# Performance work log

Hardware: AMD Instinct MI355X
Metric: run time of the kernel (lower is better)

The kernel has to match this reference:

```python
import jax, jax.numpy as jnp
import numpy as np

NUM_NODES = 100000
EMB_DIM = 256
HID_DIM = 256
NUM_REL = 500
NUM_EDGES = 250000


def setup_inputs() -> dict:
    key = jax.random.key(0)
    ks = jax.random.split(key, 6)
    x = jax.random.normal(ks[0], (NUM_NODES, EMB_DIM), dtype=jnp.float32)
    edge_index = jax.random.randint(ks[1], (2, NUM_EDGES), 0, NUM_NODES, dtype=jnp.int64)
    edge_type = jax.random.randint(ks[2], (NUM_EDGES,), 0, NUM_REL, dtype=jnp.int64)
    # nn.Linear weights: shape [out, in]; _init_weights -> normal(0,1), bias zero
    W_head = jax.random.normal(ks[3], (HID_DIM, EMB_DIM), dtype=jnp.float32)
    b_head = jnp.zeros((HID_DIM,), dtype=jnp.float32)
    W_tail = jax.random.normal(ks[4], (HID_DIM, EMB_DIM), dtype=jnp.float32)
    b_tail = jnp.zeros((HID_DIM,), dtype=jnp.float32)
    rel_emb = jax.random.normal(ks[5], (NUM_REL, HID_DIM), dtype=jnp.float32)
    return {"x": x, "edge_index": edge_index, "edge_type": edge_type,
            "W_head": W_head, "b_head": b_head,
            "W_tail": W_tail, "b_tail": b_tail, "rel_emb": rel_emb}


def reference(x, edge_index, edge_type, W_head, b_head, W_tail, b_tail, rel_emb):
    # gcn == 'no' branch of DistMultNet.forward
    h_head = x[edge_index[0]] @ W_head.T + b_head          # [E, H]
    h_tail = x[edge_index[1]] @ W_tail.T + b_tail          # [E, H]
    h_rel = rel_emb[edge_type]                             # [E, H]
    scores = jnp.sum(h_head * h_rel * h_tail, axis=1)      # [E]
    return jax.nn.sigmoid(scores)
```

## Files before the change

### kernel.cpp

```cpp
#include <hip/hip_runtime.h>
#include <math.h>

#define EMB 256

typedef _Float16 half8 __attribute__((ext_vector_type(8)));
typedef float f32x4 __attribute__((ext_vector_type(4)));

__device__ __forceinline__ void gload_lds16(const void* gsrc, void* lds) {
    __builtin_amdgcn_global_load_lds(
        (const __attribute__((address_space(1))) void*)gsrc,
        (__attribute__((address_space(3))) void*)lds,
        16, 0, 0);
}

__device__ __forceinline__ void split8(const f32x4 a, const f32x4 b,
                                       half8& hi, half8& lo) {
#pragma unroll
    for (int i = 0; i < 4; ++i) {
        hi[i]     = (_Float16)a[i];
        lo[i]     = (_Float16)(a[i] - (float)hi[i]);
        hi[4 + i] = (_Float16)b[i];
        lo[4 + i] = (_Float16)(b[i] - (float)hi[4 + i]);
    }
}

__global__ void presplit_w(const float* __restrict__ Wh, const float* __restrict__ Wt,
                           _Float16* __restrict__ Whs, _Float16* __restrict__ Wts)
{
    const int g = blockIdx.x * 256 + threadIdx.x;
    const int m = g >> 5;
    const int cs = g & 31;
    const int c = cs >> 2, seg = cs & 3;
    const float* src = (m < 256) ? Wh : Wt;
    _Float16* dst    = (m < 256) ? Whs : Wts;
    const int r = m & 255;

    const float* s = src + (size_t)r * EMB + c * 32 + seg * 8;
    const f32x4 v0 = *(const f32x4*)s;
    const f32x4 v1 = *(const f32x4*)(s + 4);
    half8 hi, lo;
    split8(v0, v1, hi, lo);
    _Float16* d = dst + (size_t)r * 512 + c * 64;
    const int sw = r & 7;
    *(half8*)(d + ((seg       ^ sw) << 3)) = hi;
    *(half8*)(d + (((4 + seg) ^ sw) << 3)) = lo;
}

__global__ __launch_bounds__(256, 2)
void gemm_single(const float* __restrict__ X,
                 const _Float16* __restrict__ Whs, const _Float16* __restrict__ Wts,
                 const float* __restrict__ bh, const float* __restrict__ bt,
                 float* __restrict__ Hout, float* __restrict__ Tout,
                 int M, int nwg)
{
    __shared__ __align__(16) float    Af[2][128 * 32];
    __shared__ __align__(16) _Float16 Bf[2][128 * 64];

    const int fl = blockIdx.x;
    const int q = nwg >> 3, r = nwg & 7;
    const int xcd = fl & 7, ix = fl >> 3;
    const int wg = (xcd < r) ? xcd * (q + 1) + ix
                             : r * (q + 1) + (xcd - r) * q + ix;
    const int variant = wg & 3;
    const int m0 = (wg >> 2) << 7;
    const int n0 = (variant & 1) << 7;
    const int sel = variant >> 1;
    const _Float16* __restrict__ Ws = sel ? Wts : Whs;
    const float* __restrict__ bias  = sel ? bt : bh;
    float* __restrict__ OUT         = sel ? Tout : Hout;

    const int tid = threadIdx.x;
    const int lane = tid & 63;
    const int wv = tid >> 6;
    const int wm = (wv >> 1) << 6;
    const int wn = (wv & 1) << 6;
    const int l15 = lane & 15, l4 = lane >> 4;

    const int srow = tid >> 3;
    const int sg = tid & 7;
    int aSrcOff[4];
    const char* bSrc0 = (const char*)Ws + (size_t)(n0 + srow) * 1024 + sg * 16;
#pragma unroll
    for (int i = 0; i < 4; ++i) {
        const int row = srow + (i << 5);
        aSrcOff[i] = (sg ^ (row & 7)) << 4;
    }
    const int ldOff = srow * 128 + sg * 16;

    f32x4 acc[4][4];
#pragma unroll
    for (int i = 0; i < 4; ++i)
#pragma unroll
        for (int j = 0; j < 4; ++j) acc[i][j] = (f32x4){0.f, 0.f, 0.f, 0.f};

    auto STAGE = [&](int b, int c) {
        const int cb = c << 7;
#pragma unroll
        for (int i = 0; i < 4; ++i) {
            const int row = srow + (i << 5);
            const int gm = m0 + row;
            const int gmc = gm < M ? gm : M - 1;
            gload_lds16((const char*)X + (size_t)gmc * 1024 + cb + aSrcOff[i],
                        (char*)&Af[b][0] + ldOff + (i << 12));
            gload_lds16(bSrc0 + (size_t)i * 32768 + cb,
                        (char*)&Bf[b][0] + ldOff + (i << 12));
        }
    };

    STAGE(0, 0);
    __syncthreads();

    for (int c = 0; c < 8; ++c) {
        const int buf = c & 1;
        if (c < 7) STAGE(buf ^ 1, c + 1);

        const char* Ab = (const char*)&Af[buf][0];
        const char* Bb = (const char*)&Bf[buf][0];

        half8 ahh[4], ahl[4];
#pragma unroll
        for (int fi = 0; fi < 4; ++fi) {
            const int row = wm + fi * 16 + l15;
            const char* rb = Ab + row * 128;
            const f32x4 a0 = *(const f32x4*)(rb + (((l4 << 1)      ^ (row & 7)) << 4));
            const f32x4 a1 = *(const f32x4*)(rb + ((((l4 << 1) | 1) ^ (row & 7)) << 4));
            split8(a0, a1, ahh[fi], ahl[fi]);
        }
#pragma unroll
        for (int j = 0; j < 4; ++j) {
            const int n = wn + j * 16 + l15;
            const int n7 = n & 7;
            const char* nb = Bb + n * 128;
            const half8 bhh = *(const half8*)(nb + (((l4    ) ^ n7) << 4));
            const half8 bhl = *(const half8*)(nb + (((l4 + 4) ^ n7) << 4));
#pragma unroll
            for (int i = 0; i < 4; ++i) {
                acc[i][j] = __builtin_amdgcn_mfma_f32_16x16x32_f16(ahh[i], bhh, acc[i][j], 0, 0, 0);
                acc[i][j] = __builtin_amdgcn_mfma_f32_16x16x32_f16(ahh[i], bhl, acc[i][j], 0, 0, 0);
                acc[i][j] = __builtin_amdgcn_mfma_f32_16x16x32_f16(ahl[i], bhh, acc[i][j], 0, 0, 0);
            }
        }
        __syncthreads();
    }

    float bv[4];
#pragma unroll
    for (int j = 0; j < 4; ++j) bv[j] = bias[n0 + wn + j * 16 + l15];

#pragma unroll
    for (int i = 0; i < 4; ++i) {
        const int rbase = m0 + wm + i * 16 + l4 * 4;
#pragma unroll
        for (int rg = 0; rg < 4; ++rg) {
            const int gr = rbase + rg;
            if (gr < M) {
                float* dst = &OUT[(size_t)gr * EMB + n0 + wn];
#pragma unroll
                for (int j = 0; j < 4; ++j)
                    dst[j * 16 + l15] = acc[i][j][rg] + bv[j];
            }
        }
    }
}

__global__ __launch_bounds__(256)
void edge_score2(const float* __restrict__ H, const float* __restrict__ T,
                 const float* __restrict__ rel, const int* __restrict__ ei,
                 const int* __restrict__ et, float* __restrict__ out, int E)
{
    const int lane = threadIdx.x & 63;
    const int wid = threadIdx.x >> 6;
    const int e0 = (blockIdx.x * 4 + wid) * 2;
    if (e0 >= E) return;
    const bool two = (e0 + 1) < E;
    const int e1 = two ? e0 + 1 : e0;

    const int s0 = ei[e0], s1 = ei[e1];
    const int d0 = ei[E + e0], d1 = ei[E + e1];
    const int r0 = et[e0], r1 = et[e1];

    const int lo = lane * 4;
    const float4 h0 = *(const float4*)&H[(size_t)s0 * EMB + lo];
    const float4 h1 = *(const float4*)&H[(size_t)s1 * EMB + lo];
    const float4 t0 = *(const float4*)&T[(size_t)d0 * EMB + lo];
    const float4 t1 = *(const float4*)&T[(size_t)d1 * EMB + lo];
    const float4 g0 = *(const float4*)&rel[(size_t)r0 * EMB + lo];
    const float4 g1 = *(const float4*)&rel[(size_t)r1 * EMB + lo];

    float p0 = h0.x * g0.x * t0.x + h0.y * g0.y * t0.y
             + h0.z * g0.z * t0.z + h0.w * g0.w * t0.w;
    float p1 = h1.x * g1.x * t1.x + h1.y * g1.y * t1.y
             + h1.z * g1.z * t1.z + h1.w * g1.w * t1.w;
#pragma unroll
    for (int off = 32; off > 0; off >>= 1) {
        p0 += __shfl_xor(p0, off, 64);
        p1 += __shfl_xor(p1, off, 64);
    }
    if (lane == 0) {
        out[e0] = 1.0f / (1.0f + expf(-p0));
        if (two) out[e1] = 1.0f / (1.0f + expf(-p1));
    }
}

__global__ __launch_bounds__(256)
void edge_direct(const float* __restrict__ X, const int* __restrict__ ei,
                 const int* __restrict__ et,
                 const float* __restrict__ Wh, const float* __restrict__ bh,
                 const float* __restrict__ Wt, const float* __restrict__ bt,
                 const float* __restrict__ rel, float* __restrict__ out, int E)
{
    __shared__ float xsrc[EMB], xdst[EMB];
    __shared__ float red[256];
    const int e = blockIdx.x;
    const int tid = threadIdx.x;
    const int src = ei[e], dst = ei[E + e], r = et[e];

    xsrc[tid] = X[(size_t)src * EMB + tid];
    xdst[tid] = X[(size_t)dst * EMB + tid];
    __syncthreads();

    float ah = 0.f, at = 0.f;
    const float* wh = Wh + (size_t)tid * EMB;
    const float* wt = Wt + (size_t)tid * EMB;
#pragma unroll 8
    for (int k = 0; k < EMB; k += 4) {
        float4 w4 = *(const float4*)&wh[k];
        ah += w4.x * xsrc[k] + w4.y * xsrc[k + 1] + w4.z * xsrc[k + 2] + w4.w * xsrc[k + 3];
        float4 v4 = *(const float4*)&wt[k];
        at += v4.x * xdst[k] + v4.y * xdst[k + 1] + v4.z * xdst[k + 2] + v4.w * xdst[k + 3];
    }
    red[tid] = (ah + bh[tid]) * rel[(size_t)r * EMB + tid] * (at + bt[tid]);
    __syncthreads();
    for (int s2 = 128; s2 > 0; s2 >>= 1) {
        if (tid < s2) red[tid] += red[tid + s2];
        __syncthreads();
    }
    if (tid == 0) out[e] = 1.0f / (1.0f + expf(-red[0]));
}

extern "C" void kernel_launch(void* const* d_in, const int* in_sizes, int n_in,
                              void* d_out, int out_size, void* d_ws, size_t ws_size,
                              hipStream_t stream) {
    const float* x   = (const float*)d_in[0];
    const int*   ei  = (const int*)d_in[1];
    const int*   et  = (const int*)d_in[2];
    const float* Wh  = (const float*)d_in[3];
    const float* bh  = (const float*)d_in[4];
    const float* Wt  = (const float*)d_in[5];
    const float* bt  = (const float*)d_in[6];
    const float* rel = (const float*)d_in[7];
    float* out = (float*)d_out;

    const int M = in_sizes[0] / EMB;
    const int E = in_sizes[2];

    const size_t szHT = (size_t)2 * M * EMB * sizeof(float);
    const size_t szWs = (size_t)2 * 256 * 512 * sizeof(_Float16);

    if (ws_size >= szHT + szWs) {
        float* H = (float*)d_ws;
        float* T = H + (size_t)M * EMB;
        _Float16* Whs = (_Float16*)((char*)d_ws + szHT);
        _Float16* Wts = Whs + (size_t)256 * 512;

        presplit_w<<<64, 256, 0, stream>>>(Wh, Wt, Whs, Wts);
        const int mtiles = (M + 127) / 128;
        const int nwg = 4 * mtiles;
        gemm_single<<<nwg, 256, 0, stream>>>(x, Whs, Wts, bh, bt, H, T, M, nwg);
        edge_score2<<<(E + 7) / 8, 256, 0, stream>>>(H, T, rel, ei, et, out, E);
    } else {
        edge_direct<<<E, 256, 0, stream>>>(x, ei, et, Wh, bh, Wt, bt, rel, out, E);
    }
}
```

Measured before the change: 217.5 us.

## Load GEMM operands directly from global to registers, score four edges per wave

```diff
diff --git a/kernel.cpp b/kernel.cpp
--- a/kernel.cpp
+++ b/kernel.cpp
@@ -5,13 +5,6 @@
 
 typedef _Float16 half8 __attribute__((ext_vector_type(8)));
 typedef float f32x4 __attribute__((ext_vector_type(4)));
-
-__device__ __forceinline__ void gload_lds16(const void* gsrc, void* lds) {
-    __builtin_amdgcn_global_load_lds(
-        (const __attribute__((address_space(1))) void*)gsrc,
-        (__attribute__((address_space(3))) void*)lds,
-        16, 0, 0);
-}
 
 __device__ __forceinline__ void split8(const f32x4 a, const f32x4 b,
                                        half8& hi, half8& lo) {
@@ -40,22 +33,18 @@
     const f32x4 v1 = *(const f32x4*)(s + 4);
     half8 hi, lo;
     split8(v0, v1, hi, lo);
-    _Float16* d = dst + (size_t)r * 512 + c * 64;
-    const int sw = r & 7;
-    *(half8*)(d + ((seg       ^ sw) << 3)) = hi;
-    *(half8*)(d + (((4 + seg) ^ sw) << 3)) = lo;
-}
-
-__global__ __launch_bounds__(256, 2)
-void gemm_single(const float* __restrict__ X,
+    _Float16* d = dst + (size_t)r * 512 + c * 64 + seg * 8;
+    *(half8*)d        = hi;
+    *(half8*)(d + 32) = lo;
+}
+
+__global__ __launch_bounds__(256, 3)
+void gemm_direct(const float* __restrict__ X,
                  const _Float16* __restrict__ Whs, const _Float16* __restrict__ Wts,
                  const float* __restrict__ bh, const float* __restrict__ bt,
                  float* __restrict__ Hout, float* __restrict__ Tout,
                  int M, int nwg)
 {
-    __shared__ __align__(16) float    Af[2][128 * 32];
-    __shared__ __align__(16) _Float16 Bf[2][128 * 64];
-
     const int fl = blockIdx.x;
     const int q = nwg >> 3, r = nwg & 7;
     const int xcd = fl & 7, ix = fl >> 3;
@@ -76,16 +65,17 @@
     const int wn = (wv & 1) << 6;
     const int l15 = lane & 15, l4 = lane >> 4;
 
-    const int srow = tid >> 3;
-    const int sg = tid & 7;
-    int aSrcOff[4];
-    const char* bSrc0 = (const char*)Ws + (size_t)(n0 + srow) * 1024 + sg * 16;
-#pragma unroll
-    for (int i = 0; i < 4; ++i) {
-        const int row = srow + (i << 5);
-        aSrcOff[i] = (sg ^ (row & 7)) << 4;
-    }
-    const int ldOff = srow * 128 + sg * 16;
+    const float* aP[4];
+#pragma unroll
+    for (int fi = 0; fi < 4; ++fi) {
+        int row = m0 + wm + fi * 16 + l15;
+        if (row >= M) row = M - 1;
+        aP[fi] = X + (size_t)row * EMB + l4 * 8;
+    }
+    const _Float16* bP[4];
+#pragma unroll
+    for (int j = 0; j < 4; ++j)
+        bP[j] = Ws + (size_t)(n0 + wn + j * 16 + l15) * 512 + l4 * 8;
 
     f32x4 acc[4][4];
 #pragma unroll
@@ -93,54 +83,28 @@
 #pragma unroll
         for (int j = 0; j < 4; ++j) acc[i][j] = (f32x4){0.f, 0.f, 0.f, 0.f};
 
-    auto STAGE = [&](int b, int c) {
-        const int cb = c << 7;
-#pragma unroll
-        for (int i = 0; i < 4; ++i) {
-            const int row = srow + (i << 5);
-            const int gm = m0 + row;
-            const int gmc = gm < M ? gm : M - 1;
-            gload_lds16((const char*)X + (size_t)gmc * 1024 + cb + aSrcOff[i],
-                        (char*)&Af[b][0] + ldOff + (i << 12));
-            gload_lds16(bSrc0 + (size_t)i * 32768 + cb,
-                        (char*)&Bf[b][0] + ldOff + (i << 12));
+#pragma unroll
+    for (int c = 0; c < 8; ++c) {
+        half8 ah[4], al[4];
+#pragma unroll
+        for (int fi = 0; fi < 4; ++fi) {
+            const float* ap = aP[fi] + c * 32;
+            const f32x4 a0 = *(const f32x4*)ap;
+            const f32x4 a1 = *(const f32x4*)(ap + 4);
+            split8(a0, a1, ah[fi], al[fi]);
         }
-    };
-
-    STAGE(0, 0);
-    __syncthreads();
-
-    for (int c = 0; c < 8; ++c) {
-        const int buf = c & 1;
-        if (c < 7) STAGE(buf ^ 1, c + 1);
-
-        const char* Ab = (const char*)&Af[buf][0];
-        const char* Bb = (const char*)&Bf[buf][0];
-
-        half8 ahh[4], ahl[4];
-#pragma unroll
-        for (int fi = 0; fi < 4; ++fi) {
-            const int row = wm + fi * 16 + l15;
-            const char* rb = Ab + row * 128;
-            const f32x4 a0 = *(const f32x4*)(rb + (((l4 << 1)      ^ (row & 7)) << 4));
-            const f32x4 a1 = *(const f32x4*)(rb + ((((l4 << 1) | 1) ^ (row & 7)) << 4));
-            split8(a0, a1, ahh[fi], ahl[fi]);
-        }
 #pragma unroll
         for (int j = 0; j < 4; ++j) {
-            const int n = wn + j * 16 + l15;
-            const int n7 = n & 7;
-            const char* nb = Bb + n * 128;
-            const half8 bhh = *(const half8*)(nb + (((l4    ) ^ n7) << 4));
-            const half8 bhl = *(const half8*)(nb + (((l4 + 4) ^ n7) << 4));
+            const _Float16* bp = bP[j] + c * 64;
+            const half8 bh8 = *(const half8*)bp;
+            const half8 bl8 = *(const half8*)(bp + 32);
 #pragma unroll
             for (int i = 0; i < 4; ++i) {
-                acc[i][j] = __builtin_amdgcn_mfma_f32_16x16x32_f16(ahh[i], bhh, acc[i][j], 0, 0, 0);
-                acc[i][j] = __builtin_amdgcn_mfma_f32_16x16x32_f16(ahh[i], bhl, acc[i][j], 0, 0, 0);
-                acc[i][j] = __builtin_amdgcn_mfma_f32_16x16x32_f16(ahl[i], bhh, acc[i][j], 0, 0, 0);
+                acc[i][j] = __builtin_amdgcn_mfma_f32_16x16x32_f16(ah[i], bh8, acc[i][j], 0, 0, 0);
+                acc[i][j] = __builtin_amdgcn_mfma_f32_16x16x32_f16(ah[i], bl8, acc[i][j], 0, 0, 0);
+                acc[i][j] = __builtin_amdgcn_mfma_f32_16x16x32_f16(al[i], bh8, acc[i][j], 0, 0, 0);
             }
         }
-        __syncthreads();
     }
 
     float bv[4];
@@ -164,41 +128,46 @@
 }
 
 __global__ __launch_bounds__(256)
-void edge_score2(const float* __restrict__ H, const float* __restrict__ T,
+void edge_score4(const float* __restrict__ H, const float* __restrict__ T,
                  const float* __restrict__ rel, const int* __restrict__ ei,
                  const int* __restrict__ et, float* __restrict__ out, int E)
 {
     const int lane = threadIdx.x & 63;
     const int wid = threadIdx.x >> 6;
-    const int e0 = (blockIdx.x * 4 + wid) * 2;
-    if (e0 >= E) return;
-    const bool two = (e0 + 1) < E;
-    const int e1 = two ? e0 + 1 : e0;
-
-    const int s0 = ei[e0], s1 = ei[e1];
-    const int d0 = ei[E + e0], d1 = ei[E + e1];
-    const int r0 = et[e0], r1 = et[e1];
+    const int base = (blockIdx.x * 4 + wid) * 4;
+    if (base >= E) return;
+
+    int e[4];
+#pragma unroll
+    for (int u = 0; u < 4; ++u) {
+        int eu = base + u;
+        e[u] = eu < E ? eu : E - 1;
+    }
 
     const int lo = lane * 4;
-    const float4 h0 = *(const float4*)&H[(size_t)s0 * EMB + lo];
-    const float4 h1 = *(const float4*)&H[(size_t)s1 * EMB + lo];
-    const float4 t0 = *(const float4*)&T[(size_t)d0 * EMB + lo];
-    const float4 t1 = *(const float4*)&T[(size_t)d1 * EMB + lo];
-    const float4 g0 = *(const float4*)&rel[(size_t)r0 * EMB + lo];
-    const float4 g1 = *(const float4*)&rel[(size_t)r1 * EMB + lo];
-
-    float p0 = h0.x * g0.x * t0.x + h0.y * g0.y * t0.y
-             + h0.z * g0.z * t0.z + h0.w * g0.w * t0.w;
-    float p1 = h1.x * g1.x * t1.x + h1.y * g1.y * t1.y
-             + h1.z * g1.z * t1.z + h1.w * g1.w * t1.w;
+    float4 h[4], t[4], g[4];
+#pragma unroll
+    for (int u = 0; u < 4; ++u) h[u] = *(const float4*)&H[(size_t)ei[e[u]] * EMB + lo];
+#pragma unroll
+    for (int u = 0; u < 4; ++u) t[u] = *(const float4*)&T[(size_t)ei[E + e[u]] * EMB + lo];
+#pragma unroll
+    for (int u = 0; u < 4; ++u) g[u] = *(const float4*)&rel[(size_t)et[e[u]] * EMB + lo];
+
+    float p[4];
+#pragma unroll
+    for (int u = 0; u < 4; ++u)
+        p[u] = h[u].x * g[u].x * t[u].x + h[u].y * g[u].y * t[u].y
+             + h[u].z * g[u].z * t[u].z + h[u].w * g[u].w * t[u].w;
+
 #pragma unroll
     for (int off = 32; off > 0; off >>= 1) {
-        p0 += __shfl_xor(p0, off, 64);
-        p1 += __shfl_xor(p1, off, 64);
+#pragma unroll
+        for (int u = 0; u < 4; ++u) p[u] += __shfl_xor(p[u], off, 64);
     }
     if (lane == 0) {
-        out[e0] = 1.0f / (1.0f + expf(-p0));
-        if (two) out[e1] = 1.0f / (1.0f + expf(-p1));
+#pragma unroll
+        for (int u = 0; u < 4; ++u)
+            out[e[u]] = 1.0f / (1.0f + expf(-p[u]));
     }
 }
 
@@ -266,8 +235,8 @@
         presplit_w<<<64, 256, 0, stream>>>(Wh, Wt, Whs, Wts);
         const int mtiles = (M + 127) / 128;
         const int nwg = 4 * mtiles;
-        gemm_single<<<nwg, 256, 0, stream>>>(x, Whs, Wts, bh, bt, H, T, M, nwg);
-        edge_score2<<<(E + 7) / 8, 256, 0, stream>>>(H, T, rel, ei, et, out, E);
+        gemm_direct<<<nwg, 256, 0, stream>>>(x, Whs, Wts, bh, bt, H, T, M, nwg);
+        edge_score4<<<(E + 15) / 16, 256, 0, stream>>>(H, T, rel, ei, et, out, E);
     } else {
         edge_direct<<<E, 256, 0, stream>>>(x, ei, et, Wh, bh, Wt, bt, rel, out, E);
     }
```

Result: slower. 304.2 us (+39.8%).
